# Optimization experiments

Measured on AMD Instinct MI355X. Metric: run time of the kernel, lower is better.

The kernel has to match this reference:

```python
import jax, jax.numpy as jnp
import numpy as np

N_HEADS = 16
D_MODEL = 1024


def setup_inputs() -> dict:
    key = jax.random.key(0)
    ks = jax.random.split(key, 9)
    B, S, D = 2, 2048, D_MODEL
    scale = 1.0 / np.sqrt(D)
    inp = {
        "x": jax.random.normal(ks[0], (B, S, D), dtype=jnp.float32),
        "wq": jax.random.normal(ks[1], (D, D), dtype=jnp.float32) * scale,
        "bq": jax.random.normal(ks[2], (D,), dtype=jnp.float32) * 0.01,
        "wk": jax.random.normal(ks[3], (D, D), dtype=jnp.float32) * scale,
        "bk": jax.random.normal(ks[4], (D,), dtype=jnp.float32) * 0.01,
        "wv": jax.random.normal(ks[5], (D, D), dtype=jnp.float32) * scale,
        "bv": jax.random.normal(ks[6], (D,), dtype=jnp.float32) * 0.01,
        "wo": jax.random.normal(ks[7], (D, D), dtype=jnp.float32) * scale,
        "bo": jax.random.normal(ks[8], (D,), dtype=jnp.float32) * 0.01,
    }
    return inp


def reference(x, wq, bq, wk, bk, wv, bv, wo, bo):
    B, S, D = x.shape
    H = N_HEADS
    hd = D // H
    # projections -> [B, H, S, hd]
    def proj(w, b):
        return (x @ w + b).reshape(B, S, H, hd).transpose(0, 2, 1, 3)
    q = proj(wq, bq)
    k = proj(wk, bk)
    v = proj(wv, bv)
    scores = jnp.einsum("bhqd,bhkd->bhqk", q, k) * (1.0 / np.sqrt(hd))
    # causal mask: future tokens (col > row) -> -inf
    causal = jnp.tril(jnp.ones((S, S), dtype=bool))  # True = allowed
    scores = jnp.where(causal[None, None, :, :], scores, -jnp.inf)
    att = jax.nn.softmax(scores, axis=-1)
    y = jnp.einsum("bhqk,bhkd->bhqd", att, v)  # [B,H,S,hd]
    y = y.transpose(0, 2, 1, 3).reshape(B, S, D)
    return y @ wo + bo
```

## Files before the change

### kernel.cpp

```cpp
#include <hip/hip_runtime.h>
#include <hip/hip_bf16.h>
#include <math.h>

typedef unsigned short u16;
typedef __bf16 bf16x8 __attribute__((ext_vector_type(8)));
typedef short s16x4 __attribute__((ext_vector_type(4)));
typedef float f32x4 __attribute__((ext_vector_type(4)));
typedef u16 u16x8 __attribute__((ext_vector_type(8)));
typedef u16 u16x4 __attribute__((ext_vector_type(4)));

#define DM 1024
#define NH 16
#define SL 2048
#define BB 2
#define TOK (BB * SL)

__device__ __forceinline__ u16 f2bf(float f) {
  union { float f; unsigned u; } v; v.f = f;
  unsigned r = v.u + 0x7FFFu + ((v.u >> 16) & 1u);
  return (u16)(r >> 16);
}

__device__ __forceinline__ float fexp2(float x) {
  float r; asm("v_exp_f32 %0, %1" : "=v"(r) : "v"(x)); return r;
}

__device__ __forceinline__ unsigned cvtpk(float lo, float hi) {
  unsigned r;
  asm("v_cvt_pk_bf16_f32 %0, %1, %2" : "=v"(r) : "v"(lo), "v"(hi));
  return r;
}

__device__ __forceinline__ f32x4 pv_mfma(s16x4 a, s16x4 b, f32x4 c) {
#if __has_builtin(__builtin_amdgcn_mfma_f32_16x16x16bf16_1k)
  return __builtin_amdgcn_mfma_f32_16x16x16bf16_1k(a, b, c, 0, 0, 0);
#else
  asm("v_mfma_f32_16x16x16_bf16 %0, %1, %2, %0" : "+v"(c) : "v"(a), "v"(b));
  return c;
#endif
}

typedef __attribute__((address_space(1))) const unsigned GU;
typedef __attribute__((address_space(3))) unsigned LU;
#define GLOAD16(g, l) __builtin_amdgcn_global_load_lds((GU*)(g), (LU*)(l), 16, 0, 0)

__global__ void cast_bf16(const float* __restrict__ in, u16* __restrict__ out, int n) {
  int i = (blockIdx.x * blockDim.x + threadIdx.x) * 8;
  if (i + 8 <= n) {
    float4 a = *(const float4*)(in + i);
    float4 b = *(const float4*)(in + i + 4);
    u16x8 o;
    o[0]=f2bf(a.x); o[1]=f2bf(a.y); o[2]=f2bf(a.z); o[3]=f2bf(a.w);
    o[4]=f2bf(b.x); o[5]=f2bf(b.y); o[6]=f2bf(b.z); o[7]=f2bf(b.w);
    *(u16x8*)(out + i) = o;
  }
}

__global__ __launch_bounds__(256) void transpose_cast4(
    const float* __restrict__ w0, const float* __restrict__ w1,
    const float* __restrict__ w2, const float* __restrict__ w3,
    u16* __restrict__ out) {
  __shared__ u16 T[64][72];
  int mat = blockIdx.z;
  const float* in = (mat == 0) ? w0 : (mat == 1) ? w1 : (mat == 2) ? w2 : w3;
  u16* o = out + ((size_t)mat << 20);
  int k0 = blockIdx.x * 64, n0 = blockIdx.y * 64;
  int tid = threadIdx.x;
  int r = tid >> 2;
  int c0 = (tid & 3) * 16;
#pragma unroll
  for (int j = 0; j < 16; j += 4) {
    float4 f = *(const float4*)(in + (size_t)(k0 + r) * 1024 + n0 + c0 + j);
    T[c0 + j + 0][r] = f2bf(f.x);
    T[c0 + j + 1][r] = f2bf(f.y);
    T[c0 + j + 2][r] = f2bf(f.z);
    T[c0 + j + 3][r] = f2bf(f.w);
  }
  __syncthreads();
  int n = tid >> 2, k1 = (tid & 3) * 16;
#pragma unroll
  for (int j = 0; j < 16; j += 8)
    *(u16x8*)(o + (size_t)(n0 + n) * 1024 + k0 + k1 + j) = *(const u16x8*)&T[n][k1 + j];
}

template<int MODE>
__global__ __launch_bounds__(256) void gemm_qkv(
    const u16* __restrict__ A, const u16* __restrict__ Bt,
    const float* __restrict__ b0, const float* __restrict__ b1,
    const float* __restrict__ b2,
    u16* __restrict__ Qo, u16* __restrict__ Ko, u16* __restrict__ Vto,
    float* __restrict__ Fo)
{
  __shared__ u16 As[3][128 * 32];
  __shared__ u16 Bs[3][128 * 32];
  const int tid = threadIdx.x, lane = tid & 63, w = tid >> 6;
  const int fr = lane & 15, fq = lane >> 4;
  const int wr = w >> 1, wc = w & 1;
  const int m0 = blockIdx.x * 128;
  const int n0 = blockIdx.y * 128;
  f32x4 acc[4][4] = {};

  auto stage = [&](int buf, int k0) {
#pragma unroll
    for (int i = 0; i < 2; ++i) {
      int b16 = i * 256 + tid;
      int row = b16 >> 2, ch = b16 & 3;
      GLOAD16(A + (size_t)(m0 + row) * DM + k0 + ((ch ^ (row & 3)) * 8), &As[buf][b16 * 8]);
    }
#pragma unroll
    for (int i = 0; i < 2; ++i) {
      int b16 = i * 256 + tid;
      int row = b16 >> 2, ch = b16 & 3;
      GLOAD16(Bt + (size_t)(n0 + row) * DM + k0 + ((ch ^ (row & 3)) * 8), &Bs[buf][b16 * 8]);
    }
  };

  const int NK = DM / 32;
  stage(0, 0);
  stage(1, 32);
  for (int j = 0; j < NK; ++j) {
    if (j + 1 < NK) asm volatile("s_waitcnt vmcnt(4)" ::: "memory");
    else            asm volatile("s_waitcnt vmcnt(0)" ::: "memory");
    __builtin_amdgcn_s_barrier();
    __builtin_amdgcn_sched_barrier(0);

    const u16* Al = As[j % 3];
    const u16* Bl = Bs[j % 3];
    bf16x8 av[4], bv[4];
#pragma unroll
    for (int m = 0; m < 4; ++m) {
      int row = wr * 64 + m * 16 + fr;
      av[m] = *(const bf16x8*)&Al[row * 32 + ((fq ^ (row & 3)) * 8)];
    }
#pragma unroll
    for (int n = 0; n < 4; ++n) {
      int row = wc * 64 + n * 16 + fr;
      bv[n] = *(const bf16x8*)&Bl[row * 32 + ((fq ^ (row & 3)) * 8)];
    }
    __builtin_amdgcn_s_setprio(1);
#pragma unroll
    for (int m = 0; m < 4; ++m)
#pragma unroll
      for (int n = 0; n < 4; ++n)
        acc[m][n] = __builtin_amdgcn_mfma_f32_16x16x32_bf16(av[m], bv[n], acc[m][n], 0, 0, 0);
    __builtin_amdgcn_s_setprio(0);

    if (j + 2 < NK) stage((j + 2) % 3, (j + 2) * 32);
  }

  if (MODE == 0) {
    int nloc = n0 & 1023;
    int mat = n0 >> 10;
    const float* bias = (mat == 0) ? b0 : ((mat == 1) ? b1 : b2);
    const float scl = (mat == 0) ? 0.18033688f : 1.0f;
#pragma unroll
    for (int m = 0; m < 4; ++m) {
      int row = m0 + wr * 64 + m * 16 + fq * 4;
#pragma unroll
      for (int n = 0; n < 4; ++n) {
        int col = nloc + wc * 64 + n * 16 + fr;
        float bc = bias[col];
        if (mat == 2) {
          u16x4 v4;
#pragma unroll
          for (int r = 0; r < 4; ++r) v4[r] = f2bf(acc[m][n][r] + bc);
          *(u16x4*)(Vto + (size_t)col * TOK + row) = v4;
        } else {
          u16* dst = (mat == 0) ? Qo : Ko;
#pragma unroll
          for (int r = 0; r < 4; ++r)
            dst[(size_t)(row + r) * DM + col] = f2bf((acc[m][n][r] + bc) * scl);
        }
      }
    }
  } else {
#pragma unroll
    for (int m = 0; m < 4; ++m) {
      int row = m0 + wr * 64 + m * 16 + fq * 4;
#pragma unroll
      for (int n = 0; n < 4; ++n) {
        int col = n0 + wc * 64 + n * 16 + fr;
        float bc = b0[col];
#pragma unroll
        for (int r = 0; r < 4; ++r)
          Fo[(size_t)(row + r) * DM + col] = acc[m][n][r] + bc;
      }
    }
  }
}

__global__ __launch_bounds__(256, 4) void attn_kernel(
    const u16* __restrict__ Qg, const u16* __restrict__ Kg,
    const u16* __restrict__ Vt, u16* __restrict__ Og)
{
  __shared__ u16 SM[16384];
  const int tid = threadIdx.x, lane = tid & 63, w = tid >> 6;
  const int fr = lane & 15, fq = lane >> 4;
  const int bid = blockIdx.x;
  const int bh = bid & 31;
  const int g = (bid >> 5) & 7;
  const int kq = bid >> 8;
  const int qt = (kq == 0) ? (31 - g) : (kq == 1) ? (16 + g)
               : (kq == 2) ? (15 - g) : g;
  const int b = bh >> 4, h = bh & 15;
  const size_t rowbase = (size_t)b * SL;
  const int nt = qt + 1;

  const int qrow = qt * 64 + w * 16 + fr;
  bf16x8 qa[2];
#pragma unroll
  for (int c = 0; c < 2; ++c)
    qa[c] = *(const bf16x8*)(Qg + (rowbase + qrow) * DM + h * 64 + c * 32 + fq * 8);

  float mrow = -INFINITY, lsum = 0.f;
  f32x4 o[4] = {};

  auto stage = [&](int buf, int t) {
#pragma unroll
    for (int i = 0; i < 2; ++i) {
      int b16 = i * 256 + tid;
      int row = b16 >> 3, ch = b16 & 7;
      GLOAD16(Kg + (rowbase + t * 64 + row) * DM + h * 64 + ((ch ^ (row & 7)) * 8),
              &SM[buf * 4096 + b16 * 8]);
    }
#pragma unroll
    for (int i = 0; i < 2; ++i) {
      int b16 = i * 256 + tid;
      int row = b16 >> 3, ch = b16 & 7;
      GLOAD16(Vt + (size_t)(h * 64 + row) * TOK + b * SL + t * 64 + ((ch ^ (row & 7)) * 8),
              &SM[8192 + buf * 4096 + b16 * 8]);
    }
  };

  stage(0, 0);
  __syncthreads();
  int buf = 0;

  for (int t = 0; t < nt; ++t) {
    if (t + 1 < nt) stage(buf ^ 1, t + 1);
    const u16* Kl = &SM[buf * 4096];
    const u16* Vl = &SM[8192 + buf * 4096];

    f32x4 st[4];
    __builtin_amdgcn_s_setprio(1);
#pragma unroll
    for (int kb = 0; kb < 4; ++kb) {
      int row = kb * 16 + fr;
      bf16x8 kf0 = *(const bf16x8*)&Kl[row * 64 + ((fq ^ (row & 7)) * 8)];
      bf16x8 kf1 = *(const bf16x8*)&Kl[row * 64 + (((4 + fq) ^ (row & 7)) * 8)];
      f32x4 s0 = {};
      s0 = __builtin_amdgcn_mfma_f32_16x16x32_bf16(kf0, qa[0], s0, 0, 0, 0);
      st[kb] = __builtin_amdgcn_mfma_f32_16x16x32_bf16(kf1, qa[1], s0, 0, 0, 0);
    }
    __builtin_amdgcn_s_setprio(0);

    if (t == qt) {
      const int kvb = t * 64 + fq * 4;
#pragma unroll
      for (int kb = 0; kb < 4; ++kb)
#pragma unroll
        for (int r = 0; r < 4; ++r)
          if (kvb + kb * 16 + r > qrow) st[kb][r] = -INFINITY;
    }

    float pm = st[0][0];
#pragma unroll
    for (int kb = 0; kb < 4; ++kb)
#pragma unroll
      for (int r = 0; r < 4; ++r) pm = fmaxf(pm, st[kb][r]);
    pm = fmaxf(pm, __shfl_xor(pm, 16, 64));
    pm = fmaxf(pm, __shfl_xor(pm, 32, 64));

    if (__any(pm > mrow + 8.f)) {
      float nm = fmaxf(mrow, pm);
      float alpha = fexp2(mrow - nm);
      mrow = nm;
      lsum *= alpha;
#pragma unroll
      for (int db = 0; db < 4; ++db)
#pragma unroll
        for (int r = 0; r < 4; ++r) o[db][r] *= alpha;
    }

    unsigned pk2[4][2];
    float ps = 0.f;
#pragma unroll
    for (int kb = 0; kb < 4; ++kb) {
      float p0 = fexp2(st[kb][0] - mrow);
      float p1 = fexp2(st[kb][1] - mrow);
      float p2 = fexp2(st[kb][2] - mrow);
      float p3 = fexp2(st[kb][3] - mrow);
      ps += (p0 + p1) + (p2 + p3);
      pk2[kb][0] = cvtpk(p0, p1);
      pk2[kb][1] = cvtpk(p2, p3);
    }
    lsum += ps;

    __builtin_amdgcn_s_setprio(1);
#pragma unroll
    for (int kb = 0; kb < 4; ++kb) {
      union { unsigned u[2]; s16x4 s; } bb;
      bb.u[0] = pk2[kb][0]; bb.u[1] = pk2[kb][1];
#pragma unroll
      for (int db = 0; db < 4; ++db) {
        int row = db * 16 + fr;
        s16x4 vfr = *(const s16x4*)&Vl[row * 64 + (((kb * 2 + (fq >> 1)) ^ (row & 7)) * 8) + ((fq & 1) * 4)];
        o[db] = pv_mfma(vfr, bb.s, o[db]);
      }
    }
    __builtin_amdgcn_s_setprio(0);

    __syncthreads();
    buf ^= 1;
  }

  float L = lsum;
  L += __shfl_xor(L, 16, 64);
  L += __shfl_xor(L, 32, 64);
  float inv = 1.0f / L;

  u16* Tb = &SM[w * 1152];
#pragma unroll
  for (int db = 0; db < 4; ++db)
#pragma unroll
    for (int w2 = 0; w2 < 2; ++w2) {
      unsigned pk = cvtpk(o[db][2 * w2] * inv, o[db][2 * w2 + 1] * inv);
      *(unsigned*)&Tb[fr * 72 + db * 16 + fq * 4 + 2 * w2] = pk;
    }
  int rr = lane >> 2, cc = (lane & 3) * 16;
  size_t gbase = (rowbase + qt * 64 + w * 16 + rr) * DM + h * 64 + cc;
#pragma unroll
  for (int j2 = 0; j2 < 2; ++j2)
    *(u16x8*)(Og + gbase + j2 * 8) = *(const u16x8*)&Tb[rr * 72 + cc + j2 * 8];
}

extern "C" void kernel_launch(void* const* d_in, const int* in_sizes, int n_in,
                              void* d_out, int out_size, void* d_ws, size_t ws_size,
                              hipStream_t stream) {
  const float* x  = (const float*)d_in[0];
  const float* wq = (const float*)d_in[1];
  const float* bq = (const float*)d_in[2];
  const float* wk = (const float*)d_in[3];
  const float* bk = (const float*)d_in[4];
  const float* wv = (const float*)d_in[5];
  const float* bv = (const float*)d_in[6];
  const float* wo = (const float*)d_in[7];
  const float* bo = (const float*)d_in[8];

  char* ws = (char*)d_ws;
  u16* Xb   = (u16*)ws;
  u16* Wall = (u16*)(ws + 8u  * 1024 * 1024);
  u16* Qb   = (u16*)(ws + 16u * 1024 * 1024);
  u16* Kb   = (u16*)(ws + 24u * 1024 * 1024);
  u16* VtG  = (u16*)(ws + 32u * 1024 * 1024);

  const int nX = TOK * DM;
  hipLaunchKernelGGL(cast_bf16, dim3(nX / (256 * 8)), dim3(256), 0, stream, x, Xb, nX);
  hipLaunchKernelGGL(transpose_cast4, dim3(16, 16, 4), dim3(256), 0, stream, wq, wk, wv, wo, Wall);

  hipLaunchKernelGGL((gemm_qkv<0>), dim3(TOK / 128, 3072 / 128), dim3(256), 0, stream,
                     Xb, Wall, bq, bk, bv, Qb, Kb, VtG, (float*)nullptr);

  hipLaunchKernelGGL(attn_kernel, dim3(32 * BB * NH), dim3(256), 0, stream,
                     Qb, Kb, VtG, Xb);

  hipLaunchKernelGGL((gemm_qkv<1>), dim3(TOK / 128, DM / 128), dim3(256), 0, stream,
                     Xb, Wall + 3u * (1u << 20), bo, (const float*)nullptr, (const float*)nullptr,
                     (u16*)nullptr, (u16*)nullptr, (u16*)nullptr, (float*)d_out);
}
```

Before: 106.4 us.

## Fuse prep kernels, shrink output-GEMM tile, compute softmax row sums via MFMA

The x cast and the four-weight transpose-cast become one prep kernel, removing a launch. The output projection GEMM gets a BM template parameter and runs with 64-row tiles, doubling its block count to 512 to fill more CUs. In attention, the per-lane row-sum accumulation and cross-lane shuffles are replaced by an extra MFMA against a vector of ones, and the row max uses max3-style reductions. The extra MFMA per key block adds matrix work, and the row sum now comes from bf16-rounded probabilities, a small accuracy shift.

```diff
diff --git a/kernel.cpp b/kernel.cpp
--- a/kernel.cpp
+++ b/kernel.cpp
@@ -29,6 +29,10 @@
   unsigned r;
   asm("v_cvt_pk_bf16_f32 %0, %1, %2" : "=v"(r) : "v"(lo), "v"(hi));
   return r;
+}
+
+__device__ __forceinline__ float max3f(float a, float b, float c) {
+  return fmaxf(fmaxf(a, b), c);
 }
 
 __device__ __forceinline__ f32x4 pv_mfma(s16x4 a, s16x4 b, f32x4 c) {
@@ -44,46 +48,47 @@
 typedef __attribute__((address_space(3))) unsigned LU;
 #define GLOAD16(g, l) __builtin_amdgcn_global_load_lds((GU*)(g), (LU*)(l), 16, 0, 0)
 
-__global__ void cast_bf16(const float* __restrict__ in, u16* __restrict__ out, int n) {
-  int i = (blockIdx.x * blockDim.x + threadIdx.x) * 8;
-  if (i + 8 <= n) {
-    float4 a = *(const float4*)(in + i);
-    float4 b = *(const float4*)(in + i + 4);
+__global__ __launch_bounds__(256) void prep(
+    const float* __restrict__ x,
+    const float* __restrict__ w0, const float* __restrict__ w1,
+    const float* __restrict__ w2, const float* __restrict__ w3,
+    u16* __restrict__ Xb, u16* __restrict__ Wall) {
+  __shared__ u16 T[64][72];
+  int bid = blockIdx.x;
+  int tid = threadIdx.x;
+  if (bid < 1024) {
+    int mat = bid >> 8;
+    const float* in = (mat == 0) ? w0 : (mat == 1) ? w1 : (mat == 2) ? w2 : w3;
+    u16* o = Wall + ((size_t)mat << 20);
+    int t2 = bid & 255;
+    int k0 = (t2 & 15) * 64, n0 = (t2 >> 4) * 64;
+    int r = tid >> 2;
+    int c0 = (tid & 3) * 16;
+#pragma unroll
+    for (int j = 0; j < 16; j += 4) {
+      float4 f = *(const float4*)(in + (size_t)(k0 + r) * 1024 + n0 + c0 + j);
+      T[c0 + j + 0][r] = f2bf(f.x);
+      T[c0 + j + 1][r] = f2bf(f.y);
+      T[c0 + j + 2][r] = f2bf(f.z);
+      T[c0 + j + 3][r] = f2bf(f.w);
+    }
+    __syncthreads();
+    int n = tid >> 2, k1 = (tid & 3) * 16;
+#pragma unroll
+    for (int j = 0; j < 16; j += 8)
+      *(u16x8*)(o + (size_t)(n0 + n) * 1024 + k0 + k1 + j) = *(const u16x8*)&T[n][k1 + j];
+  } else {
+    int i = ((bid - 1024) * 256 + tid) * 8;
+    float4 a = *(const float4*)(x + i);
+    float4 b = *(const float4*)(x + i + 4);
     u16x8 o;
     o[0]=f2bf(a.x); o[1]=f2bf(a.y); o[2]=f2bf(a.z); o[3]=f2bf(a.w);
     o[4]=f2bf(b.x); o[5]=f2bf(b.y); o[6]=f2bf(b.z); o[7]=f2bf(b.w);
-    *(u16x8*)(out + i) = o;
+    *(u16x8*)(Xb + i) = o;
   }
 }
 
-__global__ __launch_bounds__(256) void transpose_cast4(
-    const float* __restrict__ w0, const float* __restrict__ w1,
-    const float* __restrict__ w2, const float* __restrict__ w3,
-    u16* __restrict__ out) {
-  __shared__ u16 T[64][72];
-  int mat = blockIdx.z;
-  const float* in = (mat == 0) ? w0 : (mat == 1) ? w1 : (mat == 2) ? w2 : w3;
-  u16* o = out + ((size_t)mat << 20);
-  int k0 = blockIdx.x * 64, n0 = blockIdx.y * 64;
-  int tid = threadIdx.x;
-  int r = tid >> 2;
-  int c0 = (tid & 3) * 16;
-#pragma unroll
-  for (int j = 0; j < 16; j += 4) {
-    float4 f = *(const float4*)(in + (size_t)(k0 + r) * 1024 + n0 + c0 + j);
-    T[c0 + j + 0][r] = f2bf(f.x);
-    T[c0 + j + 1][r] = f2bf(f.y);
-    T[c0 + j + 2][r] = f2bf(f.z);
-    T[c0 + j + 3][r] = f2bf(f.w);
-  }
-  __syncthreads();
-  int n = tid >> 2, k1 = (tid & 3) * 16;
-#pragma unroll
-  for (int j = 0; j < 16; j += 8)
-    *(u16x8*)(o + (size_t)(n0 + n) * 1024 + k0 + k1 + j) = *(const u16x8*)&T[n][k1 + j];
-}
-
-template<int MODE>
+template<int MODE, int BM>
 __global__ __launch_bounds__(256) void gemm_qkv(
     const u16* __restrict__ A, const u16* __restrict__ Bt,
     const float* __restrict__ b0, const float* __restrict__ b1,
@@ -91,18 +96,19 @@
     u16* __restrict__ Qo, u16* __restrict__ Ko, u16* __restrict__ Vto,
     float* __restrict__ Fo)
 {
-  __shared__ u16 As[3][128 * 32];
+  constexpr int MREP = BM / 32;
+  __shared__ u16 As[3][BM * 32];
   __shared__ u16 Bs[3][128 * 32];
   const int tid = threadIdx.x, lane = tid & 63, w = tid >> 6;
   const int fr = lane & 15, fq = lane >> 4;
   const int wr = w >> 1, wc = w & 1;
-  const int m0 = blockIdx.x * 128;
+  const int m0 = blockIdx.x * BM;
   const int n0 = blockIdx.y * 128;
-  f32x4 acc[4][4] = {};
+  f32x4 acc[MREP][4] = {};
 
   auto stage = [&](int buf, int k0) {
 #pragma unroll
-    for (int i = 0; i < 2; ++i) {
+    for (int i = 0; i < BM / 64; ++i) {
       int b16 = i * 256 + tid;
       int row = b16 >> 2, ch = b16 & 3;
       GLOAD16(A + (size_t)(m0 + row) * DM + k0 + ((ch ^ (row & 3)) * 8), &As[buf][b16 * 8]);
@@ -119,17 +125,21 @@
   stage(0, 0);
   stage(1, 32);
   for (int j = 0; j < NK; ++j) {
-    if (j + 1 < NK) asm volatile("s_waitcnt vmcnt(4)" ::: "memory");
-    else            asm volatile("s_waitcnt vmcnt(0)" ::: "memory");
+    if (j + 1 < NK) {
+      if constexpr (BM == 128) asm volatile("s_waitcnt vmcnt(4)" ::: "memory");
+      else                     asm volatile("s_waitcnt vmcnt(3)" ::: "memory");
+    } else {
+      asm volatile("s_waitcnt vmcnt(0)" ::: "memory");
+    }
     __builtin_amdgcn_s_barrier();
     __builtin_amdgcn_sched_barrier(0);
 
     const u16* Al = As[j % 3];
     const u16* Bl = Bs[j % 3];
-    bf16x8 av[4], bv[4];
-#pragma unroll
-    for (int m = 0; m < 4; ++m) {
-      int row = wr * 64 + m * 16 + fr;
+    bf16x8 av[MREP], bv[4];
+#pragma unroll
+    for (int m = 0; m < MREP; ++m) {
+      int row = wr * (BM / 2) + m * 16 + fr;
       av[m] = *(const bf16x8*)&Al[row * 32 + ((fq ^ (row & 3)) * 8)];
     }
 #pragma unroll
@@ -139,7 +149,7 @@
     }
     __builtin_amdgcn_s_setprio(1);
 #pragma unroll
-    for (int m = 0; m < 4; ++m)
+    for (int m = 0; m < MREP; ++m)
 #pragma unroll
       for (int n = 0; n < 4; ++n)
         acc[m][n] = __builtin_amdgcn_mfma_f32_16x16x32_bf16(av[m], bv[n], acc[m][n], 0, 0, 0);
@@ -154,8 +164,8 @@
     const float* bias = (mat == 0) ? b0 : ((mat == 1) ? b1 : b2);
     const float scl = (mat == 0) ? 0.18033688f : 1.0f;
 #pragma unroll
-    for (int m = 0; m < 4; ++m) {
-      int row = m0 + wr * 64 + m * 16 + fq * 4;
+    for (int m = 0; m < MREP; ++m) {
+      int row = m0 + wr * (BM / 2) + m * 16 + fq * 4;
 #pragma unroll
       for (int n = 0; n < 4; ++n) {
         int col = nloc + wc * 64 + n * 16 + fr;
@@ -175,8 +185,8 @@
     }
   } else {
 #pragma unroll
-    for (int m = 0; m < 4; ++m) {
-      int row = m0 + wr * 64 + m * 16 + fq * 4;
+    for (int m = 0; m < MREP; ++m) {
+      int row = m0 + wr * (BM / 2) + m * 16 + fq * 4;
 #pragma unroll
       for (int n = 0; n < 4; ++n) {
         int col = n0 + wc * 64 + n * 16 + fr;
@@ -212,7 +222,13 @@
   for (int c = 0; c < 2; ++c)
     qa[c] = *(const bf16x8*)(Qg + (rowbase + qrow) * DM + h * 64 + c * 32 + fq * 8);
 
-  float mrow = -INFINITY, lsum = 0.f;
+  s16x4 ones1;
+  { union { u16 u[4]; s16x4 s; } t1;
+    t1.u[0] = 0x3F80; t1.u[1] = 0x3F80; t1.u[2] = 0x3F80; t1.u[3] = 0x3F80;
+    ones1 = t1.s; }
+
+  float mrow = -INFINITY;
+  f32x4 osum = {};
   f32x4 o[4] = {};
 
   auto stage = [&](int buf, int t) {
@@ -263,11 +279,12 @@
           if (kvb + kb * 16 + r > qrow) st[kb][r] = -INFINITY;
     }
 
-    float pm = st[0][0];
-#pragma unroll
-    for (int kb = 0; kb < 4; ++kb)
-#pragma unroll
-      for (int r = 0; r < 4; ++r) pm = fmaxf(pm, st[kb][r]);
+    float pa = max3f(st[0][0], st[0][1], st[0][2]);
+    float pb = max3f(st[0][3], st[1][0], st[1][1]);
+    float pc = max3f(st[1][2], st[1][3], st[2][0]);
+    float pd = max3f(st[2][1], st[2][2], st[2][3]);
+    float pe = max3f(st[3][0], st[3][1], st[3][2]);
+    float pm = max3f(max3f(pa, pb, pc), max3f(pd, pe, st[3][3]), -INFINITY);
     pm = fmaxf(pm, __shfl_xor(pm, 16, 64));
     pm = fmaxf(pm, __shfl_xor(pm, 32, 64));
 
@@ -275,7 +292,8 @@
       float nm = fmaxf(mrow, pm);
       float alpha = fexp2(mrow - nm);
       mrow = nm;
-      lsum *= alpha;
+#pragma unroll
+      for (int r = 0; r < 4; ++r) osum[r] *= alpha;
 #pragma unroll
       for (int db = 0; db < 4; ++db)
 #pragma unroll
@@ -283,24 +301,22 @@
     }
 
     unsigned pk2[4][2];
-    float ps = 0.f;
 #pragma unroll
     for (int kb = 0; kb < 4; ++kb) {
       float p0 = fexp2(st[kb][0] - mrow);
       float p1 = fexp2(st[kb][1] - mrow);
       float p2 = fexp2(st[kb][2] - mrow);
       float p3 = fexp2(st[kb][3] - mrow);
-      ps += (p0 + p1) + (p2 + p3);
       pk2[kb][0] = cvtpk(p0, p1);
       pk2[kb][1] = cvtpk(p2, p3);
     }
-    lsum += ps;
 
     __builtin_amdgcn_s_setprio(1);
 #pragma unroll
     for (int kb = 0; kb < 4; ++kb) {
       union { unsigned u[2]; s16x4 s; } bb;
       bb.u[0] = pk2[kb][0]; bb.u[1] = pk2[kb][1];
+      osum = pv_mfma(ones1, bb.s, osum);
 #pragma unroll
       for (int db = 0; db < 4; ++db) {
         int row = db * 16 + fr;
@@ -314,10 +330,7 @@
     buf ^= 1;
   }
 
-  float L = lsum;
-  L += __shfl_xor(L, 16, 64);
-  L += __shfl_xor(L, 32, 64);
-  float inv = 1.0f / L;
+  float inv = 1.0f / osum[0];
 
   u16* Tb = &SM[w * 1152];
 #pragma unroll
@@ -354,17 +367,16 @@
   u16* Kb   = (u16*)(ws + 24u * 1024 * 1024);
   u16* VtG  = (u16*)(ws + 32u * 1024 * 1024);
 
-  const int nX = TOK * DM;
-  hipLaunchKernelGGL(cast_bf16, dim3(nX / (256 * 8)), dim3(256), 0, stream, x, Xb, nX);
-  hipLaunchKernelGGL(transpose_cast4, dim3(16, 16, 4), dim3(256), 0, stream, wq, wk, wv, wo, Wall);
-
-  hipLaunchKernelGGL((gemm_qkv<0>), dim3(TOK / 128, 3072 / 128), dim3(256), 0, stream,
+  hipLaunchKernelGGL(prep, dim3(1024 + 2048), dim3(256), 0, stream,
+                     x, wq, wk, wv, wo, Xb, Wall);
+
+  hipLaunchKernelGGL((gemm_qkv<0, 128>), dim3(TOK / 128, 3072 / 128), dim3(256), 0, stream,
                      Xb, Wall, bq, bk, bv, Qb, Kb, VtG, (float*)nullptr);
 
   hipLaunchKernelGGL(attn_kernel, dim3(32 * BB * NH), dim3(256), 0, stream,
                      Qb, Kb, VtG, Xb);
 
-  hipLaunchKernelGGL((gemm_qkv<1>), dim3(TOK / 128, DM / 128), dim3(256), 0, stream,
+  hipLaunchKernelGGL((gemm_qkv<1, 64>), dim3(TOK / 64, DM / 128), dim3(256), 0, stream,
                      Xb, Wall + 3u * (1u << 20), bo, (const float*)nullptr, (const float*)nullptr,
                      (u16*)nullptr, (u16*)nullptr, (u16*)nullptr, (float*)d_out);
 }
```

After: 101.0 us, median of 3. 1.05x faster.
